# Optimization experiments

Hardware: AMD Instinct MI355X
Metric: run time of the kernel (lower is better)

## Reference

```python
import jax, jax.numpy as jnp
import numpy as np

B, Q, H, NH, HD = 2, 1024, 2048, 16, 128
QKV_ALPHA = 1e-4   # W8A8B8O8Linear output scale (a)
QKV_BETA = 1.0     # W8A8B8O8Linear bias scale (b)
QK_SCALE = 1e-4    # BMM_S8T_S8N_F32T dequant scale
PV_SCALE = 2e-3    # BMM_S8T_S8N_S8T output scale
DENSE_ALPHA = 1e-5 # W8A8BFP32OFP32Linear dequant scale
INV_NORM = 1.0 / (HD ** 0.5)


def setup_inputs() -> dict:
    key = jax.random.key(0)
    ks = jax.random.split(key, 8)
    hidden_states = jax.random.randint(ks[0], (B, Q, H), -128, 128, dtype=jnp.int32)  # int8 activations
    residual = jax.random.normal(ks[1], (B, Q, H), dtype=jnp.float32)
    alibi = jax.random.normal(ks[2], (B * NH, 1, Q), dtype=jnp.float32) * 0.1
    causal = jnp.triu(jnp.ones((Q, Q), dtype=bool), k=1)  # True = masked (future positions)
    attention_mask = jnp.broadcast_to(causal[None, None], (B, 1, Q, Q))
    w_qkv = jax.random.randint(ks[3], (3 * H, H), -128, 128, dtype=jnp.int32)   # int8 weight
    b_qkv = jax.random.randint(ks[4], (3 * H,), -128, 128, dtype=jnp.int32)     # int8 bias
    w_dense = jax.random.randint(ks[5], (H, H), -128, 128, dtype=jnp.int32)     # int8 weight
    b_dense = jax.random.normal(ks[6], (H,), dtype=jnp.float32)                 # fp32 bias
    return dict(hidden_states=hidden_states, residual=residual, alibi=alibi,
                attention_mask=attention_mask, w_qkv=w_qkv, b_qkv=b_qkv,
                w_dense=w_dense, b_dense=b_dense)


def _quant_i8(x_f32):
    return jnp.clip(jnp.round(x_f32), -128, 127).astype(jnp.int32)


def reference(hidden_states, residual, alibi, attention_mask, w_qkv, b_qkv, w_dense, b_dense):
    # --- W8A8B8O8 fused QKV linear: int8 in, int8 out ---
    acc = jnp.einsum('bqh,oh->bqo', hidden_states, w_qkv)  # exact int32 accumulation
    fused_qkv = _quant_i8(acc.astype(jnp.float32) * QKV_ALPHA + b_qkv.astype(jnp.float32) * QKV_BETA)
    # _split_heads: [B,Q,3H] -> [B,Q,NH,3,HD]
    qkv = fused_qkv.reshape(B, Q, NH, 3, HD)
    q = qkv[..., 0, :].transpose(0, 2, 1, 3).reshape(B * NH, Q, HD)
    k = qkv[..., 1, :].transpose(0, 2, 1, 3).reshape(B * NH, Q, HD)
    v = qkv[..., 2, :].transpose(0, 2, 1, 3).reshape(B * NH, Q, HD)
    # --- BMM_S8T_S8N_F32T: int8 q @ k^T -> fp32 * scale, plus alibi bias ---
    scores_i32 = jnp.einsum('nqd,nkd->nqk', q, k)  # [B*NH,Q,KV] int32
    matmul_result = alibi * 1.0 + scores_i32.astype(jnp.float32) * QK_SCALE * INV_NORM
    attention_scores = matmul_result.reshape(B, NH, Q, Q)
    # masked softmax (True = masked)
    attn_weights = jnp.where(attention_mask, jnp.finfo(jnp.float32).min, attention_scores)
    attention_probs = jax.nn.softmax(attn_weights, axis=-1)
    # quantize probs to int8 with scale 1/127 (BMM_S8T_S8N_S8T A-side)
    p_i8 = _quant_i8(attention_probs * 127.0).reshape(B * NH, Q, Q)
    # --- BMM_S8T_S8N_S8T: int8 probs @ int8 v -> int8 context ---
    ctx_acc = jnp.einsum('nqk,nkd->nqd', p_i8, v)  # int32
    ctx_i8 = _quant_i8(ctx_acc.astype(jnp.float32) * PV_SCALE)
    # _merge_heads: [B*NH,Q,HD] -> [B,Q,H]
    ctx = ctx_i8.reshape(B, NH, Q, HD).transpose(0, 2, 1, 3).reshape(B, Q, H)
    # --- W8A8BFP32OFP32 dense: int8 in, fp32 out ---
    dense_acc = jnp.einsum('bqh,oh->bqo', ctx, w_dense)
    output = dense_acc.astype(jnp.float32) * DENSE_ALPHA + b_dense + residual
    return output
```

## Files before the change

### kernel.cpp

```cpp
#include <hip/hip_runtime.h>
#include <stdint.h>

typedef int i32x4 __attribute__((ext_vector_type(4)));

#define DEV __device__ __forceinline__

DEV void glds16(const void* g, void* l) {
  __builtin_amdgcn_global_load_lds(
      (const __attribute__((address_space(1))) void*)g,
      (__attribute__((address_space(3))) void*)l, 16, 0, 0);
}

DEV int clampi8(float f) {
  int v = (int)rintf(f);
  return v < -128 ? -128 : (v > 127 ? 127 : v);
}

__global__ void pack_all_kernel(const int* __restrict__ s0, const int* __restrict__ s1,
                                const int* __restrict__ s2, int8_t* __restrict__ d0,
                                int8_t* __restrict__ d1, int8_t* __restrict__ d2) {
  const int i = blockIdx.x * 256 + threadIdx.x;
  const int* s;
  int8_t* d;
  int j;
  if (i < 1048576) { s = s0; d = d0; j = i; }
  else if (i < 4194304) { s = s1; d = d1; j = i - 1048576; }
  else { s = s2; d = d2; j = i - 4194304; }
  int4 v = ((const int4*)s)[j];
  char4 c;
  c.x = (char)v.x; c.y = (char)v.y; c.z = (char)v.z; c.w = (char)v.w;
  ((char4*)d)[j] = c;
}

__global__ __launch_bounds__(256) void qkv_kernel(
    const int8_t* __restrict__ hs8, const int8_t* __restrict__ w8,
    const int* __restrict__ bq, int8_t* __restrict__ qb, int8_t* __restrict__ kb,
    int8_t* __restrict__ vT) {
  __shared__ __align__(16) char lA[24576];
  __shared__ __align__(16) char lB[24576];
  const int l = threadIdx.x & 63, w = threadIdx.x >> 6;
  const int wm = w >> 1, wn = w & 1;
  const int lr = l & 15, lg = l >> 4;
  const int row0 = blockIdx.y * 128, col0 = blockIdx.x * 128;
  const int8_t* pA0 = hs8 + (size_t)(row0 + (w * 2 + 0) * 16 + lr) * 2048 + lg * 16;
  const int8_t* pA1 = hs8 + (size_t)(row0 + (w * 2 + 1) * 16 + lr) * 2048 + lg * 16;
  const int8_t* pB0 = w8  + (size_t)(col0 + (w * 2 + 0) * 16 + lr) * 2048 + lg * 16;
  const int8_t* pB1 = w8  + (size_t)(col0 + (w * 2 + 1) * 16 + lr) * 2048 + lg * 16;
#define QKV_STAGE(s)                                          \
  {                                                           \
    const int off_ = ((s) % 3) * 8192;                        \
    const int kk_ = (s) * 64;                                 \
    glds16(pA0 + kk_, lA + off_ + (w * 2 + 0) * 1024);        \
    glds16(pA1 + kk_, lA + off_ + (w * 2 + 1) * 1024);        \
    glds16(pB0 + kk_, lB + off_ + (w * 2 + 0) * 1024);        \
    glds16(pB1 + kk_, lB + off_ + (w * 2 + 1) * 1024);        \
  }
  QKV_STAGE(0);
  QKV_STAGE(1);
  i32x4 acc[4][4] = {};
  for (int k = 0; k < 32; ++k) {
    if (k < 31) {
      asm volatile("s_waitcnt vmcnt(4)" ::: "memory");
    } else {
      asm volatile("s_waitcnt vmcnt(0)" ::: "memory");
    }
    __builtin_amdgcn_s_barrier();
    if (k + 2 < 32) QKV_STAGE(k + 2);
    const int off = (k % 3) * 8192;
    i32x4 a[4], b[4];
#pragma unroll
    for (int i = 0; i < 4; ++i)
      a[i] = *(const i32x4*)(lA + off + ((wm * 4 + i) * 64 + l) * 16);
#pragma unroll
    for (int j = 0; j < 4; ++j)
      b[j] = *(const i32x4*)(lB + off + ((wn * 4 + j) * 64 + l) * 16);
#pragma unroll
    for (int i = 0; i < 4; ++i)
#pragma unroll
      for (int j = 0; j < 4; ++j)
        acc[i][j] = __builtin_amdgcn_mfma_i32_16x16x64_i8(a[i], b[j], acc[i][j], 0, 0, 0);
  }
#undef QKV_STAGE
#pragma unroll
  for (int j = 0; j < 4; ++j) {
    const int col = col0 + (wn * 4 + j) * 16 + lr;
    const float bias = (float)bq[col];
    const int nh = col / 384, rem = col - nh * 384;
    const int s = rem >> 7, d = rem & 127;
#pragma unroll
    for (int i = 0; i < 4; ++i) {
#pragma unroll
      for (int r = 0; r < 4; ++r) {
        const int row = row0 + (wm * 4 + i) * 16 + lg * 4 + r;
        const int bb = row >> 10, qpos = row & 1023;
        const int n = bb * 16 + nh;
        const int8_t c = (int8_t)clampi8((float)acc[i][j][r] * 1e-4f + bias);
        if (s == 0)      qb[((size_t)n << 17) + (qpos << 7) + d] = c;
        else if (s == 1) kb[((size_t)n << 17) + (qpos << 7) + d] = c;
        else             vT[((size_t)n << 17) + (d << 10) + qpos] = c;
      }
    }
  }
}

__global__ __launch_bounds__(256) void attn_stats_kernel(
    const int8_t* __restrict__ qb, const int8_t* __restrict__ kb,
    const float* __restrict__ alibi, float* __restrict__ stats) {
  const int n = blockIdx.y;
  const int tri = blockIdx.x;
  int qt = 0;
  while ((qt + 1) * (qt + 2) / 2 <= tri) ++qt;
  const int kt = tri - qt * (qt + 1) / 2;
  const int l = threadIdx.x & 63, w = threadIdx.x >> 6;
  const int lr = l & 15, lg = l >> 4;
  const int row0 = qt * 128;
  const int8_t* Qh = qb + ((size_t)n << 17);
  const int8_t* Kh = kb + ((size_t)n << 17);
  const float* al = alibi + n * 1024;

  i32x4 qa[2][2];
#pragma unroll
  for (int t = 0; t < 2; ++t)
#pragma unroll
    for (int ks = 0; ks < 2; ++ks)
      qa[t][ks] = *(const i32x4*)(Qh + (size_t)(row0 + (w * 2 + t) * 16 + lr) * 128 + ks * 64 + lg * 16);

  float sf[2][8][4];
#pragma unroll
  for (int nf = 0; nf < 8; ++nf) {
    const size_t krow = (size_t)(kt * 128 + nf * 16 + lr) * 128;
    const i32x4 bk0 = *(const i32x4*)(Kh + krow + lg * 16);
    const i32x4 bk1 = *(const i32x4*)(Kh + krow + 64 + lg * 16);
    const int col = kt * 128 + nf * 16 + lr;
    const float av = al[col];
#pragma unroll
    for (int t = 0; t < 2; ++t) {
      i32x4 sa = {0, 0, 0, 0};
      sa = __builtin_amdgcn_mfma_i32_16x16x64_i8(qa[t][0], bk0, sa, 0, 0, 0);
      sa = __builtin_amdgcn_mfma_i32_16x16x64_i8(qa[t][1], bk1, sa, 0, 0, 0);
#pragma unroll
      for (int r = 0; r < 4; ++r) {
        const int rowg = row0 + (w * 2 + t) * 16 + lg * 4 + r;
        sf[t][nf][r] = (col <= rowg)
            ? av + ((float)sa[r] * 1e-4f) * 0.08838834764831843f
            : -INFINITY;
      }
    }
  }
#pragma unroll
  for (int t = 0; t < 2; ++t)
#pragma unroll
    for (int r = 0; r < 4; ++r) {
      float tm = sf[t][0][r];
#pragma unroll
      for (int nf = 1; nf < 8; ++nf) tm = fmaxf(tm, sf[t][nf][r]);
#pragma unroll
      for (int o = 1; o < 16; o <<= 1) tm = fmaxf(tm, __shfl_xor(tm, o));
      float es = 0.f;
#pragma unroll
      for (int nf = 0; nf < 8; ++nf) es += __expf(sf[t][nf][r] - tm);
#pragma unroll
      for (int o = 1; o < 16; o <<= 1) es += __shfl_xor(es, o);
      if (lr == 0) {
        const int rowl = (w * 2 + t) * 16 + lg * 4 + r;
        float2* st = (float2*)stats;
        st[((n * 8 + qt) * 8 + kt) * 128 + rowl] = make_float2(tm, es);
      }
    }
}

__global__ __launch_bounds__(256) void attn_pv_kernel(
    const int8_t* __restrict__ qb, const int8_t* __restrict__ kb,
    const int8_t* __restrict__ vT, const float* __restrict__ alibi,
    const float* __restrict__ stats, int* __restrict__ slab0,
    int* __restrict__ slab1, int8_t* __restrict__ ctx) {
  __shared__ __align__(16) char lK[16384];
  __shared__ __align__(16) char lV[16384];
  __shared__ __align__(16) char lP[128 * 144];
  const int n = blockIdx.y, gi = blockIdx.x;
  const int sched[12] = {0x407, 0x847, 0x406, 0x403, 0x746, 0x305,
                         0x635, 0x304, 0x302, 0x534, 0x201, 0x100};
  const int s_ = sched[gi];
  const int qt = s_ & 15, kt0 = (s_ >> 4) & 15, kt1 = (s_ >> 8) & 15;
  const int l = threadIdx.x & 63, w = threadIdx.x >> 6;
  const int lr = l & 15, lg = l >> 4;
  const int row0 = qt * 128;
  const int8_t* Qh = qb + ((size_t)n << 17);
  const int8_t* Kh = kb + ((size_t)n << 17);
  const int8_t* Vh = vT + ((size_t)n << 17);
  const float* al = alibi + n * 1024;

  i32x4 qa[2][2];
#pragma unroll
  for (int t = 0; t < 2; ++t)
#pragma unroll
    for (int ks = 0; ks < 2; ++ks)
      qa[t][ks] = *(const i32x4*)(Qh + (size_t)(row0 + (w * 2 + t) * 16 + lr) * 128 + ks * 64 + lg * 16);

  float mrow[2][4], srow[2][4];
  const float2* st = (const float2*)stats;
#pragma unroll
  for (int t = 0; t < 2; ++t)
#pragma unroll
    for (int r = 0; r < 4; ++r) {
      const int rowl = (w * 2 + t) * 16 + lg * 4 + r;
      const int base = ((n * 8 + qt) * 8) * 128 + rowl;
      float m = -INFINITY;
      for (int k2 = 0; k2 <= qt; ++k2) m = fmaxf(m, st[base + k2 * 128].x);
      float s = 0.f;
      for (int k2 = 0; k2 <= qt; ++k2) {
        const float2 p = st[base + k2 * 128];
        s += p.y * __expf(p.x - m);
      }
      mrow[t][r] = m; srow[t][r] = s;
    }

  i32x4 pacc[2][8] = {};
  for (int kt = kt0; kt < kt1; ++kt) {
    __syncthreads();
#pragma unroll
    for (int e0 = 0; e0 < 4; ++e0) {
      const int e = w * 4 + e0, ks = e >> 3, mb = e & 7;
      glds16(Kh + (size_t)(kt * 128 + mb * 16 + lr) * 128 + ks * 64 + lg * 16, lK + e * 1024);
      glds16(Vh + (size_t)(mb * 16 + lr) * 1024 + kt * 128 + ks * 64 + lg * 16, lV + e * 1024);
    }
    __syncthreads();
#pragma unroll
    for (int nf = 0; nf < 8; ++nf) {
      const i32x4 bk0 = *(const i32x4*)(lK + nf * 1024 + l * 16);
      const i32x4 bk1 = *(const i32x4*)(lK + (8 + nf) * 1024 + l * 16);
      const int col = kt * 128 + nf * 16 + lr;
      const float av = al[col];
#pragma unroll
      for (int t = 0; t < 2; ++t) {
        i32x4 sa = {0, 0, 0, 0};
        sa = __builtin_amdgcn_mfma_i32_16x16x64_i8(qa[t][0], bk0, sa, 0, 0, 0);
        sa = __builtin_amdgcn_mfma_i32_16x16x64_i8(qa[t][1], bk1, sa, 0, 0, 0);
#pragma unroll
        for (int r = 0; r < 4; ++r) {
          const int rowl = (w * 2 + t) * 16 + lg * 4 + r;
          const int rowg = row0 + rowl;
          int p = 0;
          if (col <= rowg) {
            const float s = av + ((float)sa[r] * 1e-4f) * 0.08838834764831843f;
            p = (int)rintf(__expf(s - mrow[t][r]) / srow[t][r] * 127.0f);
          }
          lP[rowl * 144 + nf * 16 + lr] = (char)p;
        }
      }
    }
#pragma unroll
    for (int t = 0; t < 2; ++t) {
      const int rowl = (w * 2 + t) * 16 + lr;
      const i32x4 pa0 = *(const i32x4*)(lP + rowl * 144 + lg * 16);
      const i32x4 pa1 = *(const i32x4*)(lP + rowl * 144 + 64 + lg * 16);
#pragma unroll
      for (int nf = 0; nf < 8; ++nf) {
        const i32x4 vb0 = *(const i32x4*)(lV + nf * 1024 + l * 16);
        const i32x4 vb1 = *(const i32x4*)(lV + (8 + nf) * 1024 + l * 16);
        pacc[t][nf] = __builtin_amdgcn_mfma_i32_16x16x64_i8(pa0, vb0, pacc[t][nf], 0, 0, 0);
        pacc[t][nf] = __builtin_amdgcn_mfma_i32_16x16x64_i8(pa1, vb1, pacc[t][nf], 0, 0, 0);
      }
    }
  }
  const int bb = n >> 4, nh = n & 15;
  if (qt < 4) {
#pragma unroll
    for (int t = 0; t < 2; ++t)
#pragma unroll
      for (int nf = 0; nf < 8; ++nf)
#pragma unroll
        for (int r = 0; r < 4; ++r) {
          const int qpos = row0 + (w * 2 + t) * 16 + lg * 4 + r;
          const int d = nf * 16 + lr;
          ctx[((size_t)(bb * 1024 + qpos)) * 2048 + nh * 128 + d] =
              (int8_t)clampi8((float)pacc[t][nf][r] * 2e-3f);
        }
  } else {
    int* slab = kt0 ? slab1 : slab0;
#pragma unroll
    for (int t = 0; t < 2; ++t)
#pragma unroll
      for (int nf = 0; nf < 8; ++nf)
#pragma unroll
        for (int r = 0; r < 4; ++r) {
          const int qpos = row0 + (w * 2 + t) * 16 + lg * 4 + r;
          const int d = nf * 16 + lr;
          slab[(size_t)(bb * 512 + qpos - 512) * 2048 + nh * 128 + d] = pacc[t][nf][r];
        }
  }
}

__global__ void ctx_reduce_kernel(const int* __restrict__ slab0,
                                  const int* __restrict__ slab1,
                                  int8_t* __restrict__ ctx) {
  const int i = blockIdx.x * blockDim.x + threadIdx.x;
  const int4 a = ((const int4*)slab0)[i];
  const int4 b = ((const int4*)slab1)[i];
  const int elem0 = i * 4;
  const int r512 = elem0 >> 11, col = elem0 & 2047;
  const int bb = r512 >> 9, qpos = 512 + (r512 & 511);
  char4 c;
  c.x = (char)clampi8((float)(a.x + b.x) * 2e-3f);
  c.y = (char)clampi8((float)(a.y + b.y) * 2e-3f);
  c.z = (char)clampi8((float)(a.z + b.z) * 2e-3f);
  c.w = (char)clampi8((float)(a.w + b.w) * 2e-3f);
  ((char4*)ctx)[((size_t)(bb * 1024 + qpos) * 2048 + col) >> 2] = c;
}

__global__ __launch_bounds__(256) void dense_kernel(
    const int8_t* __restrict__ c8, const int8_t* __restrict__ w8,
    const float* __restrict__ bd, const float* __restrict__ res,
    float* __restrict__ out) {
  __shared__ __align__(16) char lA[16384];
  __shared__ __align__(16) char lB[8192];
  const int l = threadIdx.x & 63, w = threadIdx.x >> 6;
  const int wm = w >> 1, wn = w & 1;
  const int lr = l & 15, lg = l >> 4;
  const int row0 = blockIdx.y * 128, col0 = blockIdx.x * 64;
  const int8_t* pA0 = c8 + (size_t)(row0 + (w * 2 + 0) * 16 + lr) * 2048 + lg * 16;
  const int8_t* pA1 = c8 + (size_t)(row0 + (w * 2 + 1) * 16 + lr) * 2048 + lg * 16;
  const int8_t* pB  = w8 + (size_t)(col0 + w * 16 + lr) * 2048 + lg * 16;
  glds16(pA0, lA + (w * 2 + 0) * 1024);
  glds16(pA1, lA + (w * 2 + 1) * 1024);
  glds16(pB,  lB + w * 1024);
  __syncthreads();
  i32x4 acc[4][2] = {};
  int cur = 0;
  for (int k0 = 0; k0 < 2048; k0 += 64) {
    const int nxt = cur ^ 1;
    if (k0 + 64 < 2048) {
      glds16(pA0 + k0 + 64, lA + nxt * 8192 + (w * 2 + 0) * 1024);
      glds16(pA1 + k0 + 64, lA + nxt * 8192 + (w * 2 + 1) * 1024);
      glds16(pB + k0 + 64, lB + nxt * 4096 + w * 1024);
    }
    i32x4 a[4], b[2];
#pragma unroll
    for (int i = 0; i < 4; ++i)
      a[i] = *(const i32x4*)(lA + cur * 8192 + ((wm * 4 + i) * 64 + l) * 16);
#pragma unroll
    for (int j = 0; j < 2; ++j)
      b[j] = *(const i32x4*)(lB + cur * 4096 + ((wn * 2 + j) * 64 + l) * 16);
#pragma unroll
    for (int i = 0; i < 4; ++i)
#pragma unroll
      for (int j = 0; j < 2; ++j)
        acc[i][j] = __builtin_amdgcn_mfma_i32_16x16x64_i8(a[i], b[j], acc[i][j], 0, 0, 0);
    __syncthreads();
    cur = nxt;
  }
#pragma unroll
  for (int j = 0; j < 2; ++j) {
    const int col = col0 + (wn * 2 + j) * 16 + lr;
    const float bias = bd[col];
#pragma unroll
    for (int i = 0; i < 4; ++i) {
#pragma unroll
      for (int r = 0; r < 4; ++r) {
        const int row = row0 + (wm * 4 + i) * 16 + lg * 4 + r;
        const size_t o = (size_t)row * 2048 + col;
        out[o] = (float)acc[i][j][r] * 1e-5f + bias + res[o];
      }
    }
  }
}

extern "C" void kernel_launch(void* const* d_in, const int* in_sizes, int n_in,
                              void* d_out, int out_size, void* d_ws, size_t ws_size,
                              hipStream_t stream) {
  const int* hs = (const int*)d_in[0];
  const float* res = (const float*)d_in[1];
  const float* alibi = (const float*)d_in[2];
  const int* wqkv = (const int*)d_in[4];
  const int* bqkv = (const int*)d_in[5];
  const int* wd = (const int*)d_in[6];
  const float* bd = (const float*)d_in[7];
  float* out = (float*)d_out;
  char* ws = (char*)d_ws;

  int8_t* hs8   = (int8_t*)(ws + 0);
  int8_t* wqkv8 = (int8_t*)(ws + 4194304);
  int*    slab0 = (int*)(ws + 0);
  int*    slab1 = (int*)(ws + 8388608);
  int8_t* wd8   = (int8_t*)(ws + 16777216);
  int8_t* q8b   = (int8_t*)(ws + 20971520);
  int8_t* k8b   = (int8_t*)(ws + 25165824);
  int8_t* vT8   = (int8_t*)(ws + 29360128);
  int8_t* ctx8  = (int8_t*)(ws + 33554432);
  float*  stats = (float*)(ws + 37748736);

  pack_all_kernel<<<20480, 256, 0, stream>>>(hs, wqkv, wd, hs8, wqkv8, wd8);
  qkv_kernel<<<dim3(48, 16), 256, 0, stream>>>(hs8, wqkv8, bqkv, q8b, k8b, vT8);
  attn_stats_kernel<<<dim3(36, 32), 256, 0, stream>>>(q8b, k8b, alibi, stats);
  attn_pv_kernel<<<dim3(12, 32), 256, 0, stream>>>(q8b, k8b, vT8, alibi, stats,
                                                   slab0, slab1, ctx8);
  ctx_reduce_kernel<<<2048, 256, 0, stream>>>(slab0, slab1, ctx8);
  dense_kernel<<<dim3(32, 16), 256, 0, stream>>>(ctx8, wd8, bd, res, out);
}
```

Measured before the change: 181.6 us.

## Replace multi-stage async pipelines in QKV and dense GEMMs with single-buffered 256-wide K chunks

The QKV GEMM drops its triple-buffered async LDS pipeline, and the dense GEMM drops its double-buffered one. Both now load a 256-deep K chunk in one go, synchronize, compute four 64-wide sub-steps, and synchronize again. This cuts the number of barriers per K iteration and batches more loads per issue. The cost is that global-to-LDS loads no longer overlap MFMA compute, and LDS use per block grows, which may lower occupancy.

After: 190.4 us. 1.05x slower.

```diff
diff --git a/kernel.cpp b/kernel.cpp
--- a/kernel.cpp
+++ b/kernel.cpp
@@ -36,8 +36,8 @@
     const int8_t* __restrict__ hs8, const int8_t* __restrict__ w8,
     const int* __restrict__ bq, int8_t* __restrict__ qb, int8_t* __restrict__ kb,
     int8_t* __restrict__ vT) {
-  __shared__ __align__(16) char lA[24576];
-  __shared__ __align__(16) char lB[24576];
+  __shared__ __align__(16) char lA[32768];
+  __shared__ __align__(16) char lB[32768];
   const int l = threadIdx.x & 63, w = threadIdx.x >> 6;
   const int wm = w >> 1, wn = w & 1;
   const int lr = l & 15, lg = l >> 4;
@@ -46,41 +46,34 @@
   const int8_t* pA1 = hs8 + (size_t)(row0 + (w * 2 + 1) * 16 + lr) * 2048 + lg * 16;
   const int8_t* pB0 = w8  + (size_t)(col0 + (w * 2 + 0) * 16 + lr) * 2048 + lg * 16;
   const int8_t* pB1 = w8  + (size_t)(col0 + (w * 2 + 1) * 16 + lr) * 2048 + lg * 16;
-#define QKV_STAGE(s)                                          \
-  {                                                           \
-    const int off_ = ((s) % 3) * 8192;                        \
-    const int kk_ = (s) * 64;                                 \
-    glds16(pA0 + kk_, lA + off_ + (w * 2 + 0) * 1024);        \
-    glds16(pA1 + kk_, lA + off_ + (w * 2 + 1) * 1024);        \
-    glds16(pB0 + kk_, lB + off_ + (w * 2 + 0) * 1024);        \
-    glds16(pB1 + kk_, lB + off_ + (w * 2 + 1) * 1024);        \
-  }
-  QKV_STAGE(0);
-  QKV_STAGE(1);
   i32x4 acc[4][4] = {};
-  for (int k = 0; k < 32; ++k) {
-    if (k < 31) {
-      asm volatile("s_waitcnt vmcnt(4)" ::: "memory");
-    } else {
-      asm volatile("s_waitcnt vmcnt(0)" ::: "memory");
-    }
-    __builtin_amdgcn_s_barrier();
-    if (k + 2 < 32) QKV_STAGE(k + 2);
-    const int off = (k % 3) * 8192;
-    i32x4 a[4], b[4];
-#pragma unroll
-    for (int i = 0; i < 4; ++i)
-      a[i] = *(const i32x4*)(lA + off + ((wm * 4 + i) * 64 + l) * 16);
-#pragma unroll
-    for (int j = 0; j < 4; ++j)
-      b[j] = *(const i32x4*)(lB + off + ((wn * 4 + j) * 64 + l) * 16);
-#pragma unroll
-    for (int i = 0; i < 4; ++i)
+  for (int k0 = 0; k0 < 2048; k0 += 256) {
+    __syncthreads();
+#pragma unroll
+    for (int kq = 0; kq < 4; ++kq) {
+      const int ko = k0 + kq * 64;
+      glds16(pA0 + ko, lA + (kq * 8 + w * 2 + 0) * 1024);
+      glds16(pA1 + ko, lA + (kq * 8 + w * 2 + 1) * 1024);
+      glds16(pB0 + ko, lB + (kq * 8 + w * 2 + 0) * 1024);
+      glds16(pB1 + ko, lB + (kq * 8 + w * 2 + 1) * 1024);
+    }
+    __syncthreads();
+#pragma unroll
+    for (int kq = 0; kq < 4; ++kq) {
+      i32x4 a[4], b[4];
+#pragma unroll
+      for (int i = 0; i < 4; ++i)
+        a[i] = *(const i32x4*)(lA + ((kq * 8 + wm * 4 + i) * 64 + l) * 16);
 #pragma unroll
       for (int j = 0; j < 4; ++j)
-        acc[i][j] = __builtin_amdgcn_mfma_i32_16x16x64_i8(a[i], b[j], acc[i][j], 0, 0, 0);
-  }
-#undef QKV_STAGE
+        b[j] = *(const i32x4*)(lB + ((kq * 8 + wn * 4 + j) * 64 + l) * 16);
+#pragma unroll
+      for (int i = 0; i < 4; ++i)
+#pragma unroll
+        for (int j = 0; j < 4; ++j)
+          acc[i][j] = __builtin_amdgcn_mfma_i32_16x16x64_i8(a[i], b[j], acc[i][j], 0, 0, 0);
+    }
+  }
 #pragma unroll
   for (int j = 0; j < 4; ++j) {
     const int col = col0 + (wn * 4 + j) * 16 + lr;
@@ -312,8 +305,8 @@
     const int8_t* __restrict__ c8, const int8_t* __restrict__ w8,
     const float* __restrict__ bd, const float* __restrict__ res,
     float* __restrict__ out) {
-  __shared__ __align__(16) char lA[16384];
-  __shared__ __align__(16) char lB[8192];
+  __shared__ __align__(16) char lA[32768];
+  __shared__ __align__(16) char lB[16384];
   const int l = threadIdx.x & 63, w = threadIdx.x >> 6;
   const int wm = w >> 1, wn = w & 1;
   const int lr = l & 15, lg = l >> 4;
@@ -321,33 +314,32 @@
   const int8_t* pA0 = c8 + (size_t)(row0 + (w * 2 + 0) * 16 + lr) * 2048 + lg * 16;
   const int8_t* pA1 = c8 + (size_t)(row0 + (w * 2 + 1) * 16 + lr) * 2048 + lg * 16;
   const int8_t* pB  = w8 + (size_t)(col0 + w * 16 + lr) * 2048 + lg * 16;
-  glds16(pA0, lA + (w * 2 + 0) * 1024);
-  glds16(pA1, lA + (w * 2 + 1) * 1024);
-  glds16(pB,  lB + w * 1024);
-  __syncthreads();
   i32x4 acc[4][2] = {};
-  int cur = 0;
-  for (int k0 = 0; k0 < 2048; k0 += 64) {
-    const int nxt = cur ^ 1;
-    if (k0 + 64 < 2048) {
-      glds16(pA0 + k0 + 64, lA + nxt * 8192 + (w * 2 + 0) * 1024);
-      glds16(pA1 + k0 + 64, lA + nxt * 8192 + (w * 2 + 1) * 1024);
-      glds16(pB + k0 + 64, lB + nxt * 4096 + w * 1024);
-    }
-    i32x4 a[4], b[2];
-#pragma unroll
-    for (int i = 0; i < 4; ++i)
-      a[i] = *(const i32x4*)(lA + cur * 8192 + ((wm * 4 + i) * 64 + l) * 16);
-#pragma unroll
-    for (int j = 0; j < 2; ++j)
-      b[j] = *(const i32x4*)(lB + cur * 4096 + ((wn * 2 + j) * 64 + l) * 16);
-#pragma unroll
-    for (int i = 0; i < 4; ++i)
+  for (int k0 = 0; k0 < 2048; k0 += 256) {
+    __syncthreads();
+#pragma unroll
+    for (int kq = 0; kq < 4; ++kq) {
+      const int ko = k0 + kq * 64;
+      glds16(pA0 + ko, lA + (kq * 8 + w * 2 + 0) * 1024);
+      glds16(pA1 + ko, lA + (kq * 8 + w * 2 + 1) * 1024);
+      glds16(pB + ko,  lB + (kq * 4 + w) * 1024);
+    }
+    __syncthreads();
+#pragma unroll
+    for (int kq = 0; kq < 4; ++kq) {
+      i32x4 a[4], b[2];
+#pragma unroll
+      for (int i = 0; i < 4; ++i)
+        a[i] = *(const i32x4*)(lA + ((kq * 8 + wm * 4 + i) * 64 + l) * 16);
 #pragma unroll
       for (int j = 0; j < 2; ++j)
-        acc[i][j] = __builtin_amdgcn_mfma_i32_16x16x64_i8(a[i], b[j], acc[i][j], 0, 0, 0);
-    __syncthreads();
-    cur = nxt;
+        b[j] = *(const i32x4*)(lB + ((kq * 4 + wn * 2 + j) * 64 + l) * 16);
+#pragma unroll
+      for (int i = 0; i < 4; ++i)
+#pragma unroll
+        for (int j = 0; j < 2; ++j)
+          acc[i][j] = __builtin_amdgcn_mfma_i32_16x16x64_i8(a[i], b[j], acc[i][j], 0, 0, 0);
+    }
   }
 #pragma unroll
   for (int j = 0; j < 2; ++j) {
```
